# Kernel optimization log

Measured on AMD Instinct MI355X. Metric: run time of the kernel, lower is better.

Reference implementation:

```python
import jax, jax.numpy as jnp
import numpy as np

DIMS = 1024
HEADS = 16
HEAD_DIM = DIMS // HEADS


def setup_inputs() -> dict:
    key = jax.random.key(0)
    k_x, k_q, k_k, k_v = jax.random.split(key, 4)
    scale = 1.0 / np.sqrt(DIMS)
    return {
        "input_seq_embs": jax.random.normal(k_x, (4, 4096, DIMS), dtype=jnp.float32),
        # torch nn.Linear weights have shape (out_features, in_features)
        "W_Q": jax.random.normal(k_q, (DIMS, DIMS), dtype=jnp.float32) * scale,
        "W_K": jax.random.normal(k_k, (DIMS, DIMS), dtype=jnp.float32) * scale,
        "W_V": jax.random.normal(k_v, (DIMS, DIMS), dtype=jnp.float32) * scale,
    }


def reference(input_seq_embs, W_Q, W_K, W_V):
    B, L, d = input_seq_embs.shape
    H, hd = HEADS, HEAD_DIM
    # torch Linear: y = x @ W.T
    Q = (input_seq_embs @ W_Q.T).reshape(B, L, H, hd)
    K = (input_seq_embs @ W_K.T).reshape(B, L, H, hd)
    V = (input_seq_embs @ W_V.T).reshape(B, L, H, hd)
    # NOTE: original code does NOT move heads to dim 1, so matmuls act on
    # the trailing (H, hd) axes per token.
    # softmax(K^T) over heads axis: (B, L, hd, H)
    sK = jax.nn.softmax(jnp.swapaxes(K, -1, -2), axis=-1)
    # tran_V: (B, L, hd, hd)
    tran_V = jnp.einsum("bldh,blhe->blde", sK, V)
    # softmax(Q) over head_dim axis, then (B, L, H, hd)
    out = jnp.einsum("blhd,blde->blhe", jax.nn.softmax(Q, axis=-1), tran_V)
    return out.reshape(B, L, d)
```

## Files before the change

### kernel.cpp

```cpp
#include <hip/hip_runtime.h>
#include <stdint.h>
#include <stddef.h>

#define TOKENS 16384
#define CHUNK  8192
#define DMODEL 1024

typedef short   short8 __attribute__((ext_vector_type(8)));
typedef _Float16 half8 __attribute__((ext_vector_type(8)));
typedef float   f32x4  __attribute__((ext_vector_type(4)));
typedef unsigned short ushort_t;
typedef unsigned short us4 __attribute__((ext_vector_type(4)));

__device__ inline ushort_t f2h(float f) {
  union { _Float16 h; ushort_t u; } x; x.h = (_Float16)f; return x.u;
}
__device__ inline float h2f(ushort_t u) {
  union { _Float16 h; ushort_t u; } x; x.u = u; return (float)x.h;
}

template <typename V>
__device__ auto mfma16h_(V a, V b, f32x4 c, int)
    -> decltype(__builtin_amdgcn_mfma_f32_16x16x32_f16(a, b, c, 0, 0, 0)) {
  return __builtin_amdgcn_mfma_f32_16x16x32_f16(a, b, c, 0, 0, 0);
}
template <typename V>
__device__ f32x4 mfma16h_(V a, V b, f32x4 c, long) {
  return __builtin_amdgcn_mfma_f32_16x16x32_f16(
      __builtin_bit_cast(half8, a), __builtin_bit_cast(half8, b), c, 0, 0, 0);
}
__device__ inline f32x4 MFMA16H(short8 a, short8 b, f32x4 c) {
  return mfma16h_(a, b, c, 0);
}

__device__ inline void gload_lds16(const void* g, void* l) {
  __builtin_amdgcn_global_load_lds(
      (const __attribute__((address_space(1))) unsigned int*)g,
      (__attribute__((address_space(3))) unsigned int*)l, 16, 0, 0);
}

__device__ inline void wave_lds_fence() {
  asm volatile("s_waitcnt lgkmcnt(0)" ::: "memory");
  __builtin_amdgcn_sched_barrier(0);
}

__global__ __launch_bounds__(256) void conv_w(
    const float* __restrict__ Wq, const float* __restrict__ Wk,
    const float* __restrict__ Wv, ushort_t* __restrict__ Wh, int n4)
{
  int i = blockIdx.x * 256 + threadIdx.x;
  if (i >= n4) return;
  const float* src = (blockIdx.y == 0) ? Wq : ((blockIdx.y == 1) ? Wk : Wv);
  f32x4 x = ((const f32x4*)src)[i];
  us4 h;
  #pragma unroll
  for (int j = 0; j < 4; ++j) h[j] = f2h(x[j]);
  ((us4*)(Wh + (size_t)blockIdx.y * DMODEL * DMODEL))[i] = h;
}

__global__ __launch_bounds__(256) void conv_x(
    const float* __restrict__ src, ushort_t* __restrict__ dst, int n4)
{
  int i = blockIdx.x * 256 + threadIdx.x;
  if (i >= n4) return;
  f32x4 x = ((const f32x4*)src)[i];
  us4 h;
  #pragma unroll
  for (int j = 0; j < 4; ++j) h[j] = f2h(x[j]);
  ((us4*)dst)[i] = h;
}

__global__ __launch_bounds__(256, 4) void gemm_h(
    const ushort_t* __restrict__ Xh,
    const ushort_t* __restrict__ Wh, ushort_t* __restrict__ Y)
{
  __shared__ ushort_t Ah[128 * 32];
  __shared__ ushort_t Bh[128 * 32];

  const int tid  = threadIdx.x;
  const int lane = tid & 63;
  const int wave = tid >> 6;
  const int quad = lane >> 4;
  const int l15  = lane & 15;
  const int wm   = wave & 1, wn = wave >> 1;

  const int m0 = blockIdx.x * 128;
  const int n0 = blockIdx.y * 128;
  const int z  = blockIdx.z;

  const ushort_t* Agh = Xh + (size_t)m0 * DMODEL;
  const ushort_t* Bgh = Wh + (size_t)z * DMODEL * DMODEL + (size_t)n0 * DMODEL;
  ushort_t* Yp = Y + (size_t)z * CHUNK * DMODEL;

  const int s_row = tid >> 2;
  const int s_c3  = tid & 3;

  f32x4 acc[4][4] = {};

  const short8* Ahv = (const short8*)Ah;
  const short8* Bhv = (const short8*)Bh;

  for (int k0 = 0; k0 < DMODEL; k0 += 32) {
    #pragma unroll
    for (int p = 0; p < 2; ++p) {
      const int rowp = p * 64 + s_row;
      const int koff = (s_c3 ^ ((rowp >> 1) & 3)) * 8;
      size_t g = (size_t)rowp * DMODEL + k0 + koff;
      int ldso = (p * 256 + wave * 64) * 16;
      gload_lds16(Agh + g, (char*)Ah + ldso);
      gload_lds16(Bgh + g, (char*)Bh + ldso);
    }
    __syncthreads();

    short8 ah[4], bh[4];
    #pragma unroll
    for (int i = 0; i < 4; ++i) {
      const int row = wm * 64 + i * 16 + l15;
      ah[i] = Ahv[row * 4 + (quad ^ ((row >> 1) & 3))];
    }
    #pragma unroll
    for (int j = 0; j < 4; ++j) {
      const int row = wn * 64 + j * 16 + l15;
      bh[j] = Bhv[row * 4 + (quad ^ ((row >> 1) & 3))];
    }

    #pragma unroll
    for (int i = 0; i < 4; ++i) {
      #pragma unroll
      for (int j = 0; j < 4; ++j)
        acc[i][j] = MFMA16H(ah[i], bh[j], acc[i][j]);
    }
    __syncthreads();
  }

  #pragma unroll
  for (int i = 0; i < 4; ++i) {
    #pragma unroll
    for (int j = 0; j < 4; ++j) {
      #pragma unroll
      for (int r = 0; r < 4; ++r) {
        int row = m0 + wm * 64 + i * 16 + quad * 4 + r;
        int col = n0 + wn * 64 + j * 16 + l15;
        Yp[(size_t)row * DMODEL + col] = f2h(acc[i][j][r]);
      }
    }
  }
}

__global__ __launch_bounds__(256) void attn_mix(
    const ushort_t* __restrict__ QKV, float* __restrict__ Out)
{
  __shared__ __align__(16) ushort_t V_s[4][16 * 72];
  __shared__ __align__(16) float    M_s[4][16 * 20];

  const int tid  = threadIdx.x;
  const int lane = tid & 63;
  const int wv   = tid >> 6;
  const int tok  = blockIdx.x * 4 + wv;

  const int l15  = lane & 15;
  const int quad = lane >> 4;
  const int hrow = lane >> 3;
  const int dcol = (lane & 7) * 8;

  ushort_t* Vl = V_s[wv];
  float*    Ml = M_s[wv];

  const size_t base = (size_t)tok * DMODEL;
  const short8* Q8 = (const short8*)(QKV + base);
  const short8* K8 = (const short8*)(QKV + (size_t)CHUNK * DMODEL + base);
  const short8* V8 = (const short8*)(QKV + 2 * (size_t)CHUNK * DMODEL + base);

  short8 vra = V8[lane], vrb = V8[64 + lane];
  *(short8*)(Vl + hrow * 72 + dcol)       = vra;
  *(short8*)(Vl + (hrow + 8) * 72 + dcol) = vrb;

  const int fidx = l15 * 8 + quad;
  short8 qf0 = Q8[fidx], qf1 = Q8[fidx + 4];
  short8 kf0 = K8[fidx], kf1 = K8[fidx + 4];

  float eq0[8], eq1[8], ek0[8], ek1[8];
  #pragma unroll
  for (int j = 0; j < 8; ++j) {
    eq0[j] = __expf(h2f((ushort_t)qf0[j]));
    eq1[j] = __expf(h2f((ushort_t)qf1[j]));
    ek0[j] = __expf(h2f((ushort_t)kf0[j]));
    ek1[j] = __expf(h2f((ushort_t)kf1[j]));
  }

  float s0[8], s1[8];
  #pragma unroll
  for (int j = 0; j < 8; ++j) { s0[j] = ek0[j]; s1[j] = ek1[j]; }
  #pragma unroll
  for (int j = 0; j < 8; ++j) {
    s0[j] += __shfl_xor(s0[j], 1);
    s0[j] += __shfl_xor(s0[j], 2);
    s0[j] += __shfl_xor(s0[j], 4);
    s0[j] += __shfl_xor(s0[j], 8);
    s1[j] += __shfl_xor(s1[j], 1);
    s1[j] += __shfl_xor(s1[j], 2);
    s1[j] += __shfl_xor(s1[j], 4);
    s1[j] += __shfl_xor(s1[j], 8);
  }

  float sq = 0.f;
  #pragma unroll
  for (int j = 0; j < 8; ++j) sq += eq0[j] + eq1[j];
  sq += __shfl_xor(sq, 16);
  sq += __shfl_xor(sq, 32);
  const float invSq = __builtin_amdgcn_rcpf(sq);

  short8 a0v, a1v, b0v, b1v;
  #pragma unroll
  for (int j = 0; j < 8; ++j) {
    a0v[j] = (short)f2h(eq0[j] * (invSq * __builtin_amdgcn_rcpf(s0[j])));
    a1v[j] = (short)f2h(eq1[j] * (invSq * __builtin_amdgcn_rcpf(s1[j])));
    b0v[j] = (short)f2h(ek0[j]);
    b1v[j] = (short)f2h(ek1[j]);
  }

  f32x4 acc = {};
  acc = MFMA16H(a0v, b0v, acc);
  acc = MFMA16H(a1v, b1v, acc);

  #pragma unroll
  for (int r = 0; r < 4; ++r) Ml[(quad * 4 + r) * 20 + l15] = acc[r];

  wave_lds_fence();

  f32x4 m0[4], m1[4];
  #pragma unroll
  for (int j = 0; j < 4; ++j) {
    m0[j] = *(const f32x4*)(Ml + hrow * 20 + j * 4);
    m1[j] = *(const f32x4*)(Ml + (hrow + 8) * 20 + j * 4);
  }
  float o0[8] = {0.f, 0.f, 0.f, 0.f, 0.f, 0.f, 0.f, 0.f};
  float o1[8] = {0.f, 0.f, 0.f, 0.f, 0.f, 0.f, 0.f, 0.f};
  #pragma unroll
  for (int hp = 0; hp < 16; ++hp) {
    short8 vv = *(const short8*)(Vl + hp * 72 + dcol);
    const float w0 = m0[hp >> 2][hp & 3];
    const float w1 = m1[hp >> 2][hp & 3];
    #pragma unroll
    for (int j = 0; j < 8; ++j) {
      float vf = h2f((ushort_t)vv[j]);
      o0[j] += w0 * vf;
      o1[j] += w1 * vf;
    }
  }

  float* O0 = Out + base + hrow * 64 + dcol;
  float* O1 = Out + base + (hrow + 8) * 64 + dcol;
  f32x4 w;
  w[0] = o0[0]; w[1] = o0[1]; w[2] = o0[2]; w[3] = o0[3]; *(f32x4*)(O0)     = w;
  w[0] = o0[4]; w[1] = o0[5]; w[2] = o0[6]; w[3] = o0[7]; *(f32x4*)(O0 + 4) = w;
  w[0] = o1[0]; w[1] = o1[1]; w[2] = o1[2]; w[3] = o1[3]; *(f32x4*)(O1)     = w;
  w[0] = o1[4]; w[1] = o1[5]; w[2] = o1[6]; w[3] = o1[7]; *(f32x4*)(O1 + 4) = w;
}

extern "C" void kernel_launch(void* const* d_in, const int* in_sizes, int n_in,
                              void* d_out, int out_size, void* d_ws, size_t ws_size,
                              hipStream_t stream) {
  const float* X  = (const float*)d_in[0];
  const float* Wq = (const float*)d_in[1];
  const float* Wk = (const float*)d_in[2];
  const float* Wv = (const float*)d_in[3];
  float* Out = (float*)d_out;

  const size_t WSZ = (size_t)DMODEL * DMODEL;
  const size_t XSZ = (size_t)CHUNK * DMODEL;
  ushort_t* Wh = (ushort_t*)d_ws;
  ushort_t* Xh = Wh + 3 * WSZ;
  ushort_t* Y  = Xh + XSZ;

  const int wn4 = (int)(WSZ / 4);
  dim3 gw((wn4 + 255) / 256, 3);
  conv_w<<<gw, 256, 0, stream>>>(Wq, Wk, Wv, Wh, wn4);

  const int xn4 = (int)(XSZ / 4);
  dim3 gg(CHUNK / 128, DMODEL / 128, 3);
  for (int c = 0; c < 2; ++c) {
    conv_x<<<(xn4 + 255) / 256, 256, 0, stream>>>(X + (size_t)c * XSZ, Xh, xn4);
    gemm_h<<<gg, 256, 0, stream>>>(Xh, Wh, Y);
    attn_mix<<<CHUNK / 4, 256, 0, stream>>>(Y, Out + (size_t)c * XSZ);
  }
}
```

Before: 288.3 us.

## Use 256x256 double-buffered GEMM tiles and process all tokens in one chunk

The QKV projection GEMM moves from 128x128 tiles with BK=32 and 256 threads to 256x256 tiles with BK=64 and 512 threads. It double-buffers LDS so the next K tile loads while MFMAs run on the current one, and raises wave priority around the MFMA block. The host now runs all 16384 tokens in one pass when the workspace is large enough, which removes the second conv/gemm/attn launch round. The cost is 128KB of LDS per block, so only one block fits per CU, and higher register pressure from 128 accumulators per thread.

```diff
diff --git a/kernel.cpp b/kernel.cpp
--- a/kernel.cpp
+++ b/kernel.cpp
@@ -70,76 +70,89 @@
   ((us4*)dst)[i] = h;
 }
 
-__global__ __launch_bounds__(256, 4) void gemm_h(
-    const ushort_t* __restrict__ Xh,
-    const ushort_t* __restrict__ Wh, ushort_t* __restrict__ Y)
+__global__ __launch_bounds__(512, 2) void gemm_h(
+    const ushort_t* __restrict__ Xh, const ushort_t* __restrict__ Wh,
+    ushort_t* __restrict__ Y, int tokens)
 {
-  __shared__ ushort_t Ah[128 * 32];
-  __shared__ ushort_t Bh[128 * 32];
+  __shared__ ushort_t As[2][256 * 64];
+  __shared__ ushort_t Bs[2][256 * 64];
 
   const int tid  = threadIdx.x;
   const int lane = tid & 63;
-  const int wave = tid >> 6;
+  const int wid  = tid >> 6;
   const int quad = lane >> 4;
   const int l15  = lane & 15;
-  const int wm   = wave & 1, wn = wave >> 1;
-
-  const int m0 = blockIdx.x * 128;
-  const int n0 = blockIdx.y * 128;
+  const int wm   = wid >> 2;
+  const int wn   = wid & 3;
+
+  const int m0 = blockIdx.x * 256;
+  const int n0 = blockIdx.y * 256;
   const int z  = blockIdx.z;
 
-  const ushort_t* Agh = Xh + (size_t)m0 * DMODEL;
-  const ushort_t* Bgh = Wh + (size_t)z * DMODEL * DMODEL + (size_t)n0 * DMODEL;
-  ushort_t* Yp = Y + (size_t)z * CHUNK * DMODEL;
-
-  const int s_row = tid >> 2;
-  const int s_c3  = tid & 3;
-
-  f32x4 acc[4][4] = {};
-
-  const short8* Ahv = (const short8*)Ah;
-  const short8* Bhv = (const short8*)Bh;
-
-  for (int k0 = 0; k0 < DMODEL; k0 += 32) {
+  const ushort_t* Ag = Xh + (size_t)m0 * DMODEL;
+  const ushort_t* Bg = Wh + (size_t)z * DMODEL * DMODEL + (size_t)n0 * DMODEL;
+  ushort_t* Yp = Y + (size_t)z * tokens * DMODEL;
+
+  f32x4 acc[8][4] = {};
+
+  auto stage = [&](int t, int b) {
+    const int kbase = t * 64;
     #pragma unroll
-    for (int p = 0; p < 2; ++p) {
-      const int rowp = p * 64 + s_row;
-      const int koff = (s_c3 ^ ((rowp >> 1) & 3)) * 8;
-      size_t g = (size_t)rowp * DMODEL + k0 + koff;
-      int ldso = (p * 256 + wave * 64) * 16;
-      gload_lds16(Agh + g, (char*)Ah + ldso);
-      gload_lds16(Bgh + g, (char*)Bh + ldso);
+    for (int i = 0; i < 4; ++i) {
+      const int c    = i * 512 + tid;
+      const int row  = c >> 3;
+      const int koff = (((c & 7) ^ (row & 7)) << 3);
+      const size_t g = (size_t)row * DMODEL + kbase + koff;
+      const int ldso = (i * 512 + wid * 64) * 16;
+      gload_lds16(Ag + g, (char*)As[b] + ldso);
+      gload_lds16(Bg + g, (char*)Bs[b] + ldso);
+    }
+  };
+
+  stage(0, 0);
+  __syncthreads();
+
+  for (int t = 0; t < DMODEL / 64; ++t) {
+    const int b = t & 1;
+    if (t + 1 < DMODEL / 64) stage(t + 1, b ^ 1);
+
+    const short8* Av = (const short8*)As[b];
+    const short8* Bv = (const short8*)Bs[b];
+
+    #pragma unroll
+    for (int s = 0; s < 2; ++s) {
+      short8 ah[8], bh[4];
+      #pragma unroll
+      for (int i = 0; i < 8; ++i) {
+        const int r  = wm * 128 + i * 16 + l15;
+        const int kc = s * 4 + quad;
+        ah[i] = Av[r * 8 + (kc ^ (r & 7))];
+      }
+      #pragma unroll
+      for (int j = 0; j < 4; ++j) {
+        const int r  = wn * 64 + j * 16 + l15;
+        const int kc = s * 4 + quad;
+        bh[j] = Bv[r * 8 + (kc ^ (r & 7))];
+      }
+      __builtin_amdgcn_s_setprio(1);
+      #pragma unroll
+      for (int i = 0; i < 8; ++i) {
+        #pragma unroll
+        for (int j = 0; j < 4; ++j)
+          acc[i][j] = MFMA16H(ah[i], bh[j], acc[i][j]);
+      }
+      __builtin_amdgcn_s_setprio(0);
     }
     __syncthreads();
-
-    short8 ah[4], bh[4];
-    #pragma unroll
-    for (int i = 0; i < 4; ++i) {
-      const int row = wm * 64 + i * 16 + l15;
-      ah[i] = Ahv[row * 4 + (quad ^ ((row >> 1) & 3))];
-    }
-    #pragma unroll
-    for (int j = 0; j < 4; ++j) {
-      const int row = wn * 64 + j * 16 + l15;
-      bh[j] = Bhv[row * 4 + (quad ^ ((row >> 1) & 3))];
-    }
-
-    #pragma unroll
-    for (int i = 0; i < 4; ++i) {
-      #pragma unroll
-      for (int j = 0; j < 4; ++j)
-        acc[i][j] = MFMA16H(ah[i], bh[j], acc[i][j]);
-    }
-    __syncthreads();
-  }
-
-  #pragma unroll
-  for (int i = 0; i < 4; ++i) {
+  }
+
+  #pragma unroll
+  for (int i = 0; i < 8; ++i) {
     #pragma unroll
     for (int j = 0; j < 4; ++j) {
       #pragma unroll
       for (int r = 0; r < 4; ++r) {
-        int row = m0 + wm * 64 + i * 16 + quad * 4 + r;
+        int row = m0 + wm * 128 + i * 16 + quad * 4 + r;
         int col = n0 + wn * 64 + j * 16 + l15;
         Yp[(size_t)row * DMODEL + col] = f2h(acc[i][j][r]);
       }
@@ -148,7 +161,7 @@
 }
 
 __global__ __launch_bounds__(256) void attn_mix(
-    const ushort_t* __restrict__ QKV, float* __restrict__ Out)
+    const ushort_t* __restrict__ QKV, float* __restrict__ Out, int tokens)
 {
   __shared__ __align__(16) ushort_t V_s[4][16 * 72];
   __shared__ __align__(16) float    M_s[4][16 * 20];
@@ -167,9 +180,10 @@
   float*    Ml = M_s[wv];
 
   const size_t base = (size_t)tok * DMODEL;
+  const size_t zstr = (size_t)tokens * DMODEL;
   const short8* Q8 = (const short8*)(QKV + base);
-  const short8* K8 = (const short8*)(QKV + (size_t)CHUNK * DMODEL + base);
-  const short8* V8 = (const short8*)(QKV + 2 * (size_t)CHUNK * DMODEL + base);
+  const short8* K8 = (const short8*)(QKV + zstr + base);
+  const short8* V8 = (const short8*)(QKV + 2 * zstr + base);
 
   short8 vra = V8[lane], vrb = V8[64 + lane];
   *(short8*)(Vl + hrow * 72 + dcol)       = vra;
@@ -268,20 +282,24 @@
   float* Out = (float*)d_out;
 
   const size_t WSZ = (size_t)DMODEL * DMODEL;
-  const size_t XSZ = (size_t)CHUNK * DMODEL;
+
+  const size_t need1 = (3 * WSZ + (size_t)TOKENS * DMODEL * 4) * sizeof(ushort_t);
+  const int    nck  = (ws_size >= need1) ? 1 : 2;
+  const size_t ctok = (nck == 1) ? (size_t)TOKENS : (size_t)CHUNK;
+
   ushort_t* Wh = (ushort_t*)d_ws;
   ushort_t* Xh = Wh + 3 * WSZ;
-  ushort_t* Y  = Xh + XSZ;
+  ushort_t* Yw = Xh + ctok * DMODEL;
 
   const int wn4 = (int)(WSZ / 4);
   dim3 gw((wn4 + 255) / 256, 3);
   conv_w<<<gw, 256, 0, stream>>>(Wq, Wk, Wv, Wh, wn4);
 
-  const int xn4 = (int)(XSZ / 4);
-  dim3 gg(CHUNK / 128, DMODEL / 128, 3);
-  for (int c = 0; c < 2; ++c) {
-    conv_x<<<(xn4 + 255) / 256, 256, 0, stream>>>(X + (size_t)c * XSZ, Xh, xn4);
-    gemm_h<<<gg, 256, 0, stream>>>(Xh, Wh, Y);
-    attn_mix<<<CHUNK / 4, 256, 0, stream>>>(Y, Out + (size_t)c * XSZ);
-  }
-}
+  const int xn4 = (int)(ctok * DMODEL / 4);
+  dim3 gg((unsigned)(ctok / 256), DMODEL / 256, 3);
+  for (int c = 0; c < nck; ++c) {
+    conv_x<<<(xn4 + 255) / 256, 256, 0, stream>>>(X + c * ctok * DMODEL, Xh, xn4);
+    gemm_h<<<gg, 512, 0, stream>>>(Xh, Wh, Yw, (int)ctok);
+    attn_mix<<<(unsigned)(ctok / 4), 256, 0, stream>>>(Yw, Out + c * ctok * DMODEL, (int)ctok);
+  }
+}
```

Result: faster. 265.5 us (-7.9%).
